# Optimization experiments

Hardware: AMD Instinct MI355X
Metric: run time of the kernel (lower is better)

## Reference

```python
import jax, jax.numpy as jnp
import numpy as np

DIM = 64; Hh = 128; Ww = 128; Bz = 4
N = 8      # d_state
R = 4      # dt_rank = ceil(dim/16)
K = 4      # depthwise conv kernel
NB = 4     # number of CrossMambaBlocks (spa, spe, spa_cross, spe_cross)


def setup_inputs() -> dict:
    key = jax.random.key(0)
    ks = jax.random.split(key, 16)
    f32 = jnp.float32
    D = DIM
    rn = lambda k, shp, s: jax.random.normal(k, shp, f32) * s
    inp = {
        "img1": rn(ks[0], (Bz, D, Hh, Ww), 1.0),
        "img2": rn(ks[1], (Bz, D, Hh, Ww), 1.0),
        "img1_sum": rn(ks[2], (Bz, D, Hh, Ww), 1.0),
        "img2_sum": rn(ks[3], (Bz, D, Hh, Ww), 1.0),
        # LayerNorm params for norm0/norm1 of each block
        "ln_g0": jnp.ones((NB, D), f32), "ln_b0": jnp.zeros((NB, D), f32),
        "ln_g1": jnp.ones((NB, D), f32), "ln_b1": jnp.zeros((NB, D), f32),
        # Mamba projections (in_proj -> x,z from input0; in_proj_e -> extra embedding path)
        "W_in": rn(ks[4], (NB, D, 2 * D), D ** -0.5),
        "W_ine": rn(ks[5], (NB, D, D), D ** -0.5),
        # per-direction depthwise causal conv
        "convW": rn(ks[6], (NB, 2, D, K), K ** -0.5),
        "convB": jnp.zeros((NB, 2, D), f32),
        # x_proj (dt, B, C) computed from the cross-modal embedding (v7 cross variant)
        "W_x": rn(ks[7], (NB, 2, D, R + 2 * N), D ** -0.5),
        "W_dt": rn(ks[8], (NB, 2, R, D), R ** -0.5),
        "b_dt": jnp.full((NB, 2, D), -4.6, f32),  # softplus ~ 0.01
        "A_log": jnp.log(jnp.broadcast_to(jnp.arange(1, N + 1, dtype=f32), (NB, 2, D, N))),
        "Dp": jnp.ones((NB, 2, D), f32),
        "W_out": rn(ks[9], (NB, D, D), D ** -0.5),
        "b_out": jnp.zeros((NB, D), f32),
        # FusionMamba.out_proj
        "W_fo": rn(ks[10], (D, D), D ** -0.5),
        "b_fo": jnp.zeros((D,), f32),
    }
    return inp


def _ln(x, g, b):
    m = x.mean(-1, keepdims=True)
    v = ((x - m) ** 2).mean(-1, keepdims=True)
    return (x - m) * jax.lax.rsqrt(v + 1e-5) * g + b


def _causal_conv(x, w, b):
    # x: [B, L, D], w: [D, K] depthwise causal conv
    xt = x.transpose(0, 2, 1)  # [B, D, L]
    out = jax.lax.conv_general_dilated(xt, w[:, None, :], (1,), [(K - 1, 0)],
                                       feature_group_count=w.shape[0])
    return out.transpose(0, 2, 1) + b


def _selective_scan(x, dt, Bm, Cm, A):
    # x, dt: [B, L, D]; Bm, Cm: [B, L, N]; A: [D, N]
    def step(h, t):
        x_t, dt_t, B_t, C_t = t  # [B,D],[B,D],[B,N],[B,N]
        dA = jnp.exp(dt_t[:, :, None] * A)                       # [B,D,N]
        h = h * dA + (dt_t * x_t)[:, :, None] * B_t[:, None, :]  # [B,D,N]
        y = jnp.einsum('bdn,bn->bd', h, C_t)
        return h, y
    h0 = jnp.zeros((x.shape[0], x.shape[2], A.shape[1]), x.dtype)
    xs = (x.transpose(1, 0, 2), dt.transpose(1, 0, 2),
          Bm.transpose(1, 0, 2), Cm.transpose(1, 0, 2))
    _, ys = jax.lax.scan(step, h0, xs)
    return ys.transpose(1, 0, 2)  # [B, L, D]


def _cross_mamba_block(x0, x1, i, p):
    # x0, x1: [B, L, D]; bidirectional cross Mamba (bimamba v7, sum of directions)
    skip = x0
    a = _ln(x0, p['ln_g0'][i], p['ln_b0'][i])
    e = _ln(x1, p['ln_g1'][i], p['ln_b1'][i])
    xz = a @ p['W_in'][i]
    x, z = jnp.split(xz, 2, axis=-1)
    ee = e @ p['W_ine'][i]  # cross-modal embedding drives dt/B/C
    y = 0.0
    for d in range(2):
        xd = x if d == 0 else x[:, ::-1]
        ed = ee if d == 0 else ee[:, ::-1]
        zd = z if d == 0 else z[:, ::-1]
        xc = jax.nn.silu(_causal_conv(xd, p['convW'][i, d], p['convB'][i, d]))
        dbl = ed @ p['W_x'][i, d]
        dtr, Bm, Cm = dbl[..., :R], dbl[..., R:R + N], dbl[..., R + N:]
        dt = jax.nn.softplus(dtr @ p['W_dt'][i, d] + p['b_dt'][i, d])
        A = -jnp.exp(p['A_log'][i, d])
        yd = _selective_scan(xc, dt, Bm, Cm, A) + xc * p['Dp'][i, d]
        yd = yd * jax.nn.silu(zd)
        if d == 1:
            yd = yd[:, ::-1]
        y = y + yd
    return y @ p['W_out'][i] + p['b_out'][i] + skip


def reference(img1, img2, img1_sum, img2_sum, ln_g0, ln_b0, ln_g1, ln_b1,
              W_in, W_ine, convW, convB, W_x, W_dt, b_dt, A_log, Dp,
              W_out, b_out, W_fo, b_fo):
    p = dict(ln_g0=ln_g0, ln_b0=ln_b0, ln_g1=ln_g1, ln_b1=ln_b1, W_in=W_in,
             W_ine=W_ine, convW=convW, convB=convB, W_x=W_x, W_dt=W_dt,
             b_dt=b_dt, A_log=A_log, Dp=Dp, W_out=W_out, b_out=b_out)
    b, c, h, w = img1.shape
    flat = lambda t: t.reshape(b, c, h * w).transpose(0, 2, 1)   # b c h w -> b (hw) c
    unflat = lambda t: t.transpose(0, 2, 1).reshape(b, c, h, w)
    x1, x2, s1, s2 = flat(img1), flat(img2), flat(img1_sum), flat(img2_sum)
    x1 = _cross_mamba_block(x1, s1, 0, p)  # spa layer
    x2 = _cross_mamba_block(x2, s2, 1, p)  # spe layer
    spa = _cross_mamba_block(x1, x2, 2, p)
    spe = _cross_mamba_block(x2, x1, 3, p)
    fusion = (spa + spe) @ W_fo + b_fo
    out = unflat(fusion)
    return (unflat(x1) + out, unflat(x2) + out, img1_sum, img2_sum)
```

## Files before the change

### kernel.cpp

```cpp
#include <hip/hip_runtime.h>
#include <hip/hip_bf16.h>

#define BZ 4
#define DD 64
#define LL 16384
#define NN 8
#define BLD ((size_t)BZ*DD*LL)
#define BML ((size_t)BZ*20*LL)

__device__ __forceinline__ float silu_(float x){ return __fdividef(x, 1.f + __expf(-x)); }
__device__ __forceinline__ float softplus_(float x){ return (x > 20.f) ? x : __logf(1.f + __expf(x)); }


__global__ __launch_bounds__(256)
void k_in2(const float* __restrict__ s0a, const float* __restrict__ s1a,
           const float* __restrict__ s0b, const float* __restrict__ s1b,
           const float* __restrict__ lng0, const float* __restrict__ lnb0,
           const float* __restrict__ lng1, const float* __restrict__ lnb1,
           const float* __restrict__ W_in, const float* __restrict__ W_ine,
           const float* __restrict__ W_x, int i0,
           float* __restrict__ XBa, float* __restrict__ ZBa,
           float* __restrict__ XBb, float* __restrict__ ZBb,
           float* __restrict__ M00, float* __restrict__ M01,
           float* __restrict__ M10, float* __restrict__ M11)
{
  const int sel  = blockIdx.x >> 8;
  const int pi   = sel / 3;
  const int role = sel - 3*pi;
  const int pos = (blockIdx.x & 255)*256 + threadIdx.x;
  const int b = pos >> 14;
  const int l = pos & (LL-1);
  const int i = i0 + pi;

  if (role < 2){
    const float* src0 = pi ? s0b : s0a;
    float a[DD];
    #pragma unroll
    for (int ch=0; ch<DD; ++ch) a[ch] = src0[((size_t)(b*DD+ch))*LL + l];
    float m=0.f;
    #pragma unroll
    for (int k=0;k<DD;++k) m += a[k];
    m *= (1.f/DD);
    float v=0.f;
    #pragma unroll
    for (int k=0;k<DD;++k){ float d=a[k]-m; v += d*d; }
    v *= (1.f/DD);
    const float rs = rsqrtf(v + 1e-5f);
    #pragma unroll
    for (int k=0;k<DD;++k) a[k] = (a[k]-m)*rs*lng0[i*DD+k] + lnb0[i*DD+k];

    const float* Wi = W_in + (size_t)i*DD*2*DD;
    float* drow = ((role==0) ? (pi ? XBb : XBa) : (pi ? ZBb : ZBa)) + ((size_t)b*LL + l)*DD;
    const int gbase = role*4;
    for (int g=0; g<4; ++g){
      float acc[16];
      #pragma unroll
      for (int j=0;j<16;++j) acc[j]=0.f;
      #pragma unroll
      for (int k=0;k<DD;++k){
        const float av = a[k];
        const float* wr = Wi + k*128 + (gbase+g)*16;
        #pragma unroll
        for (int j=0;j<16;++j) acc[j] = fmaf(av, wr[j], acc[j]);
      }
      #pragma unroll
      for (int q=0;q<4;++q)
        ((float4*)(drow + g*16))[q] = make_float4(acc[4*q],acc[4*q+1],acc[4*q+2],acc[4*q+3]);
    }
  } else {
    const float* src1 = pi ? s1b : s1a;
    float e[DD];
    #pragma unroll
    for (int ch=0; ch<DD; ++ch) e[ch] = src1[((size_t)(b*DD+ch))*LL + l];
    float m=0.f;
    #pragma unroll
    for (int k=0;k<DD;++k) m += e[k];
    m *= (1.f/DD);
    float v=0.f;
    #pragma unroll
    for (int k=0;k<DD;++k){ float d=e[k]-m; v += d*d; }
    v *= (1.f/DD);
    const float rs = rsqrtf(v + 1e-5f);
    #pragma unroll
    for (int k=0;k<DD;++k) e[k] = (e[k]-m)*rs*lng1[i*DD+k] + lnb1[i*DD+k];

    const float* We  = W_ine + (size_t)i*DD*DD;
    const float* Wx0 = W_x + ((size_t)(i*2+0)*DD)*20;
    const float* Wx1 = W_x + ((size_t)(i*2+1)*DD)*20;
    float acc0[20], acc1[20];
    #pragma unroll
    for (int j=0;j<20;++j){ acc0[j]=0.f; acc1[j]=0.f; }
    for (int gg=0; gg<4; ++gg){
      float eeg[16];
      #pragma unroll
      for (int j=0;j<16;++j) eeg[j]=0.f;
      #pragma unroll
      for (int k=0;k<DD;++k){
        const float ev = e[k];
        const float* wr = We + k*DD + gg*16;
        #pragma unroll
        for (int j=0;j<16;++j) eeg[j] = fmaf(ev, wr[j], eeg[j]);
      }
      const float* w0 = Wx0 + (size_t)(gg*16)*20;
      const float* w1 = Wx1 + (size_t)(gg*16)*20;
      #pragma unroll
      for (int jj=0;jj<16;++jj){
        const float s = eeg[jj];
        #pragma unroll
        for (int j=0;j<20;++j){
          acc0[j] = fmaf(s, w0[jj*20+j], acc0[j]);
          acc1[j] = fmaf(s, w1[jj*20+j], acc1[j]);
        }
      }
    }
    float* mrow0 = (pi ? M10 : M00) + ((size_t)b*LL + l)*20;
    float* mrow1 = (pi ? M11 : M01) + ((size_t)b*LL + l)*20;
    #pragma unroll
    for (int q=0;q<5;++q){
      ((float4*)mrow0)[q] = make_float4(acc0[4*q],acc0[4*q+1],acc0[4*q+2],acc0[4*q+3]);
      ((float4*)mrow1)[q] = make_float4(acc1[4*q],acc1[4*q+1],acc1[4*q+2],acc1[4*q+3]);
    }
  }
}

template<int NC2, bool PASSC>
__global__ __launch_bounds__(64)
void k_scan4(const float* __restrict__ XBa, const float* __restrict__ XBb,
             const float* __restrict__ ZBa, const float* __restrict__ ZBb,
             float* __restrict__ Y0, float* __restrict__ Y1,
             float* __restrict__ Y2, float* __restrict__ Y3,
             const float* __restrict__ M00, const float* __restrict__ M01,
             const float* __restrict__ M10, const float* __restrict__ M11,
             const float* __restrict__ convW, const float* __restrict__ convB,
             const float* __restrict__ Wdt, const float* __restrict__ bdt,
             const float* __restrict__ Alog, const float* __restrict__ Dpw, int i0,
             float* __restrict__ PP, float* __restrict__ FF,
             const float* __restrict__ HH)
{
  const int TC2 = LL / NC2;
  const size_t SC2 = (size_t)BZ*NC2*DD*NN;
  const int inst = blockIdx.x / (BZ*NC2);
  const int rb = blockIdx.x - inst*(BZ*NC2);
  const int c = rb & (NC2-1);
  const int b = rb / NC2;
  const int ch = threadIdx.x;
  const int pi = inst >> 1, d = inst & 1;
  const int id = (i0+pi)*2 + d;

  const float* xb = pi ? XBb : XBa;
  const float* zb = pi ? ZBb : ZBa;
  const float* meta = (inst==0)?M00:(inst==1)?M01:(inst==2)?M10:M11;
  float* yb = (inst==0)?Y0:(inst==1)?Y1:(inst==2)?Y2:Y3;

  float cw[4];
  #pragma unroll
  for (int k=0;k<4;++k) cw[k] = convW[((size_t)id*DD+ch)*4 + k];
  const float cb = convB[id*DD + ch];
  float wd[4];
  #pragma unroll
  for (int r=0;r<4;++r) wd[r] = Wdt[((size_t)id*4 + r)*DD + ch];
  const float bd = bdt[id*DD + ch];
  float An[NN];
  #pragma unroll
  for (int n=0;n<NN;++n) An[n] = -__expf(Alog[((size_t)id*DD+ch)*NN + n]);
  const float dp = PASSC ? Dpw[id*DD + ch] : 0.f;

  bool fastA = true;
  #pragma unroll
  for (int n=0;n<NN;++n) fastA = fastA && (fabsf(An[n] + (float)(n+1)) < 1e-3f);

  const size_t sbase = (size_t)inst*SC2 + ((size_t)(b*NC2+c)*DD + ch)*NN;
  float h[NN], P[NN];
  float Sdt = 0.f;
  if (PASSC){
    #pragma unroll
    for (int n=0;n<NN;++n) h[n] = HH[sbase+n];
  } else {
    #pragma unroll
    for (int n=0;n<NN;++n){ h[n]=0.f; P[n]=1.f; }
  }

  const int stp = d ? -1 : 1;
  const int t0  = d ? (LL-1 - c*TC2) : (c*TC2);

  float p1=0.f, p2=0.f, p3=0.f;
  {
    int tp = t0 - stp;
    if ((unsigned)tp < LL) p1 = xb[((size_t)b*LL+tp)*DD+ch];
    tp -= stp;
    if ((unsigned)tp < LL) p2 = xb[((size_t)b*LL+tp)*DD+ch];
    tp -= stp;
    if ((unsigned)tp < LL) p3 = xb[((size_t)b*LL+tp)*DD+ch];
  }

  int t = t0;
  for (int s=0; s<TC2; ++s, t+=stp){
    const size_t row = (size_t)b*LL + t;
    const float xv = xb[row*DD+ch];
    const float xc = silu_(cb + cw[0]*p3 + cw[1]*p2 + cw[2]*p1 + cw[3]*xv);
    p3=p2; p2=p1; p1=xv;

    const float* mt = meta + row*20;
    const float dpre = bd + mt[0]*wd[0] + mt[1]*wd[1] + mt[2]*wd[2] + mt[3]*wd[3];
    const float dt = softplus_(dpre);
    const float u = dt*xc;

    float dA[NN];
    if (fastA){
      const float E = __expf(-dt);
      const float E2 = E*E, E4 = E2*E2;
      dA[0]=E;    dA[1]=E2;    dA[2]=E2*E;  dA[3]=E4;
      dA[4]=E4*E; dA[5]=E4*E2; dA[6]=E4*E2*E; dA[7]=E4*E4;
      Sdt += dt;
    } else {
      #pragma unroll
      for (int n=0;n<NN;++n) dA[n] = __expf(dt*An[n]);
    }

    if (!PASSC){
      #pragma unroll
      for (int n=0;n<NN;++n) h[n] = fmaf(h[n], dA[n], u*mt[4+n]);
      if (!fastA){
        #pragma unroll
        for (int n=0;n<NN;++n) P[n] *= dA[n];
      }
    } else {
      float y = 0.f;
      #pragma unroll
      for (int n=0;n<NN;++n){
        h[n] = fmaf(h[n], dA[n], u*mt[4+n]);
        y = fmaf(h[n], mt[12+n], y);
      }
      const float zv = zb[row*DD+ch];
      yb[row*DD + ch] = (y + xc*dp)*silu_(zv);
    }
  }

  if (!PASSC){
    if (fastA){
      const float E = __expf(-Sdt);
      const float E2 = E*E, E4 = E2*E2;
      P[0]=E;    P[1]=E2;    P[2]=E2*E;  P[3]=E4;
      P[4]=E4*E; P[5]=E4*E2; P[6]=E4*E2*E; P[7]=E4*E4;
    }
    #pragma unroll
    for (int n=0;n<NN;++n){ PP[sbase+n] = P[n]; FF[sbase+n] = h[n]; }
  }
}

template<int NC2>
__global__ __launch_bounds__(256)
void k_mid4(const float* __restrict__ PP, const float* __restrict__ FF,
            float* __restrict__ HH)
{
  const size_t SC2 = (size_t)BZ*NC2*DD*NN;
  const int inst = blockIdx.x >> 3;
  const int idx = (blockIdx.x & 7)*256 + threadIdx.x;
  const int b  = idx >> 9;
  const int cn = idx & 511;
  const size_t base = (size_t)inst*SC2;
  float h = 0.f;
  #pragma unroll 4
  for (int c=0; c<NC2; ++c){
    const size_t a2 = base + (((size_t)(b*NC2+c))<<9) + cn;
    HH[a2] = h;
    h = h*PP[a2] + FF[a2];
  }
}

__global__ __launch_bounds__(256)
void k_out2(const float* __restrict__ Y0, const float* __restrict__ Y1,
            const float* __restrict__ Y2, const float* __restrict__ Y3,
            const float* __restrict__ skipA, const float* __restrict__ skipB,
            const float* __restrict__ Wout, const float* __restrict__ bout,
            float* __restrict__ dstA, float* __restrict__ dstB)
{
  const int sel = blockIdx.x >> 8;
  const int pi = sel >> 2;
  const int g  = sel & 3;
  const int pos = (blockIdx.x & 255)*256 + threadIdx.x;
  const int b = pos >> 14;
  const int l = pos & (LL-1);
  const size_t row = ((size_t)b*LL + l)*DD;

  const float* Ya = pi ? Y2 : Y0;
  const float* Yb = pi ? Y3 : Y1;
  const float* skip = pi ? skipB : skipA;
  float* dst = pi ? dstB : dstA;
  const float* Wo = Wout + (size_t)pi*DD*DD;
  const float* bo = bout + pi*DD;

  float y[DD];
  {
    const float4* pa = (const float4*)(Ya + row);
    const float4* pb = (const float4*)(Yb + row);
    #pragma unroll
    for (int q=0;q<16;++q){
      float4 v0=pa[q], v1=pb[q];
      y[4*q]=v0.x+v1.x; y[4*q+1]=v0.y+v1.y; y[4*q+2]=v0.z+v1.z; y[4*q+3]=v0.w+v1.w;
    }
  }
  float acc[16];
  #pragma unroll
  for (int j=0;j<16;++j) acc[j]=0.f;
  #pragma unroll
  for (int k=0;k<DD;++k){
    const float av = y[k];
    const float* wr = Wo + k*DD + g*16;
    #pragma unroll
    for (int j=0;j<16;++j) acc[j] = fmaf(av, wr[j], acc[j]);
  }
  #pragma unroll
  for (int j=0;j<16;++j){
    const int col = g*16 + j;
    const size_t o = ((size_t)(b*DD+col))*LL + l;
    dst[o] = acc[j] + bo[col] + skip[o];
  }
}

__global__ __launch_bounds__(256)
void k_o34(const float* __restrict__ Y0, const float* __restrict__ Y1,
           const float* __restrict__ Y2, const float* __restrict__ Y3,
           const float* __restrict__ X1, const float* __restrict__ X2,
           const float* __restrict__ Wout, const float* __restrict__ bout,
           float* __restrict__ FSa, float* __restrict__ FSb)
{
  const int sel = blockIdx.x >> 8;
  const int wh = sel >> 2;
  const int g  = sel & 3;
  const int pos = (blockIdx.x & 255)*256 + threadIdx.x;
  const int b = pos >> 14;
  const int l = pos & (LL-1);
  const size_t row = ((size_t)b*LL + l)*DD;

  const float* Ya = wh ? Y2 : Y0;
  const float* Yb = wh ? Y3 : Y1;
  const float* skip = wh ? X2 : X1;
  float* FS = wh ? FSb : FSa;
  const float* Wo = Wout + (size_t)(2+wh)*DD*DD;
  const float* bo = bout + (2+wh)*DD;

  float y[DD];
  {
    const float4* pa = (const float4*)(Ya + row);
    const float4* pb = (const float4*)(Yb + row);
    #pragma unroll
    for (int q=0;q<16;++q){
      float4 v0=pa[q], v1=pb[q];
      y[4*q]=v0.x+v1.x; y[4*q+1]=v0.y+v1.y; y[4*q+2]=v0.z+v1.z; y[4*q+3]=v0.w+v1.w;
    }
  }
  float acc[16];
  #pragma unroll
  for (int j=0;j<16;++j) acc[j]=0.f;
  #pragma unroll
  for (int k=0;k<DD;++k){
    const float av = y[k];
    const float* wr = Wo + k*DD + g*16;
    #pragma unroll
    for (int j=0;j<16;++j) acc[j] = fmaf(av, wr[j], acc[j]);
  }
  float* frow = FS + row + g*16;
  #pragma unroll
  for (int q=0;q<4;++q){
    const int j4 = 4*q;
    make_float4(0,0,0,0);
    float4 v;
    v.x = acc[j4+0] + bo[g*16+j4+0] + skip[((size_t)(b*DD+g*16+j4+0))*LL + l];
    v.y = acc[j4+1] + bo[g*16+j4+1] + skip[((size_t)(b*DD+g*16+j4+1))*LL + l];
    v.z = acc[j4+2] + bo[g*16+j4+2] + skip[((size_t)(b*DD+g*16+j4+2))*LL + l];
    v.w = acc[j4+3] + bo[g*16+j4+3] + skip[((size_t)(b*DD+g*16+j4+3))*LL + l];
    ((float4*)frow)[q] = v;
  }
}

__global__ __launch_bounds__(256)
void k_fuse2(const float* __restrict__ FSa, const float* __restrict__ FSb,
             const float* __restrict__ X1, const float* __restrict__ X2,
             const float* __restrict__ Wfo, const float* __restrict__ bfo,
             float* __restrict__ ob)
{
  const int g = blockIdx.x >> 8;
  const int pos = (blockIdx.x & 255)*256 + threadIdx.x;
  const int b = pos >> 14;
  const int l = pos & (LL-1);
  const size_t row = ((size_t)b*LL + l)*DD;

  float fs[DD];
  {
    const float4* pa = (const float4*)(FSa + row);
    const float4* pb = (const float4*)(FSb + row);
    #pragma unroll
    for (int q=0;q<16;++q){
      float4 v0=pa[q], v1=pb[q];
      fs[4*q]=v0.x+v1.x; fs[4*q+1]=v0.y+v1.y; fs[4*q+2]=v0.z+v1.z; fs[4*q+3]=v0.w+v1.w;
    }
  }
  float acc[16];
  #pragma unroll
  for (int j=0;j<16;++j) acc[j]=0.f;
  #pragma unroll
  for (int k=0;k<DD;++k){
    const float av = fs[k];
    const float* wr = Wfo + k*DD + g*16;
    #pragma unroll
    for (int j=0;j<16;++j) acc[j] = fmaf(av, wr[j], acc[j]);
  }
  #pragma unroll
  for (int j=0;j<16;++j){
    const int col = g*16 + j;
    const size_t o = ((size_t)(b*DD+col))*LL + l;
    const float fu = acc[j] + bfo[col];
    ob[o]       = X1[o] + fu;
    ob[BLD + o] = X2[o] + fu;
  }
}

__global__ __launch_bounds__(256)
void k_copyboth(const float* __restrict__ s1, const float* __restrict__ s2,
                float* __restrict__ o)
{
  const size_t gid = (size_t)blockIdx.x*256 + threadIdx.x;
  const size_t half = BLD/4;
  if (gid < half) ((float4*)(o        ))[gid]        = ((const float4*)s1)[gid];
  else            ((float4*)(o + BLD ))[gid - half]  = ((const float4*)s2)[gid - half];
}

__global__ __launch_bounds__(256)
void k_copy4(const float* __restrict__ s, float* __restrict__ o)
{
  const size_t i = (size_t)blockIdx.x*256 + threadIdx.x;
  ((float4*)o)[i] = ((const float4*)s)[i];
}

__global__ __launch_bounds__(256)
void f_in(const float* __restrict__ src0, const float* __restrict__ src1,
          const float* __restrict__ lng0, const float* __restrict__ lnb0,
          const float* __restrict__ lng1, const float* __restrict__ lnb1,
          const float* __restrict__ W_in, const float* __restrict__ W_ine,
          const float* __restrict__ W_x, int i,
          float* __restrict__ XB, float* __restrict__ ZB,
          float* __restrict__ M0, float* __restrict__ M1)
{
  const int gid = blockIdx.x*256 + threadIdx.x;
  const int b = gid >> 14;
  const int l = gid & (LL-1);

  float a[DD];
  for (int ch=0; ch<DD; ++ch) a[ch] = src0[((size_t)(b*DD+ch))*LL + l];
  {
    float m=0.f; for (int k=0;k<DD;++k) m += a[k];  m *= (1.f/DD);
    float v=0.f; for (int k=0;k<DD;++k){ float d=a[k]-m; v += d*d; }  v *= (1.f/DD);
    float rs = rsqrtf(v + 1e-5f);
    for (int k=0;k<DD;++k) a[k] = (a[k]-m)*rs*lng0[i*DD+k] + lnb0[i*DD+k];
  }
  const float* Wi = W_in + (size_t)i*DD*2*DD;
  float* xrow = XB + ((size_t)b*LL + l)*DD;
  float* zrow = ZB + ((size_t)b*LL + l)*DD;
  for (int g=0; g<8; ++g){
    float acc[16];
    #pragma unroll
    for (int j=0;j<16;++j) acc[j]=0.f;
    for (int k=0;k<DD;++k){
      const float av = a[k];
      const float* wr = Wi + k*128 + g*16;
      #pragma unroll
      for (int j=0;j<16;++j) acc[j] = fmaf(av, wr[j], acc[j]);
    }
    float* drow = (g<4) ? (xrow + g*16) : (zrow + (g-4)*16);
    #pragma unroll
    for (int q=0;q<4;++q)
      ((float4*)drow)[q] = make_float4(acc[4*q],acc[4*q+1],acc[4*q+2],acc[4*q+3]);
  }
  float e[DD], ee[DD];
  for (int ch=0; ch<DD; ++ch) e[ch] = src1[((size_t)(b*DD+ch))*LL + l];
  {
    float m=0.f; for (int k=0;k<DD;++k) m += e[k];  m *= (1.f/DD);
    float v=0.f; for (int k=0;k<DD;++k){ float d=e[k]-m; v += d*d; }  v *= (1.f/DD);
    float rs = rsqrtf(v + 1e-5f);
    for (int k=0;k<DD;++k) e[k] = (e[k]-m)*rs*lng1[i*DD+k] + lnb1[i*DD+k];
  }
  const float* We = W_ine + (size_t)i*DD*DD;
  for (int m2=0; m2<DD; ++m2){
    float s = 0.f;
    for (int k=0;k<DD;++k) s = fmaf(e[k], We[k*DD + m2], s);
    ee[m2] = s;
  }
  for (int d=0; d<2; ++d){
    float acc[20];
    #pragma unroll
    for (int j=0;j<20;++j) acc[j]=0.f;
    for (int m2=0; m2<DD; ++m2){
      const float ev = ee[m2];
      const float* wr = W_x + ((size_t)(i*2+d)*DD + m2)*20;
      #pragma unroll
      for (int j=0;j<20;++j) acc[j] = fmaf(ev, wr[j], acc[j]);
    }
    float* mrow = (d ? M1 : M0) + ((size_t)b*LL + l)*20;
    #pragma unroll
    for (int q=0;q<5;++q)
      ((float4*)mrow)[q] = make_float4(acc[4*q],acc[4*q+1],acc[4*q+2],acc[4*q+3]);
  }
}

template<int DIR, bool PASSC>
__global__ __launch_bounds__(64)
void f_scan(const float* __restrict__ xb, const float* __restrict__ zb,
            float* __restrict__ yb, const float* __restrict__ meta,
            const float* __restrict__ convW, const float* __restrict__ convB,
            const float* __restrict__ Wdt, const float* __restrict__ bdt,
            const float* __restrict__ Alog, const float* __restrict__ Dpw, int id,
            float* __restrict__ Pb, float* __restrict__ Fb,
            const float* __restrict__ Hin)
{
  const int ch = threadIdx.x;
  const int c  = blockIdx.x & 255;
  const int b  = blockIdx.x >> 8;

  float cw[4];
  for (int k=0;k<4;++k) cw[k] = convW[((size_t)id*DD+ch)*4 + k];
  const float cb = convB[id*DD + ch];
  float wd[4]; for (int r=0;r<4;++r) wd[r] = Wdt[((size_t)id*4 + r)*DD + ch];
  const float bd = bdt[id*DD + ch];
  float An[NN]; for (int n=0;n<NN;++n) An[n] = -__expf(Alog[((size_t)id*DD+ch)*NN + n]);
  const float dp = PASSC ? Dpw[id*DD + ch] : 0.f;

  const size_t sbase = ((size_t)(b*256+c)*DD + ch)*NN;
  float h[NN], P[NN];
  if (PASSC){
    #pragma unroll
    for (int n=0;n<NN;++n) h[n] = Hin[sbase+n];
  } else {
    #pragma unroll
    for (int n=0;n<NN;++n){ h[n]=0.f; P[n]=1.f; }
  }

  int t0, stp;
  if (DIR==0){ t0 = c*64;        stp =  1; }
  else       { t0 = LL-1 - c*64; stp = -1; }

  float p1=0.f, p2=0.f, p3=0.f;
  {
    int tp = t0 - stp;
    if ((unsigned)tp < LL) p1 = xb[((size_t)b*LL+tp)*DD+ch];
    tp -= stp;
    if ((unsigned)tp < LL) p2 = xb[((size_t)b*LL+tp)*DD+ch];
    tp -= stp;
    if ((unsigned)tp < LL) p3 = xb[((size_t)b*LL+tp)*DD+ch];
  }

  int t = t0;
  for (int s=0; s<64; ++s, t+=stp){
    const size_t row = (size_t)b*LL + t;
    const float xv = xb[row*DD+ch];
    const float xc = silu_(cb + cw[0]*p3 + cw[1]*p2 + cw[2]*p1 + cw[3]*xv);
    p3=p2; p2=p1; p1=xv;

    const float* mt = meta + row*20;
    const float dpre = bd + mt[0]*wd[0] + mt[1]*wd[1] + mt[2]*wd[2] + mt[3]*wd[3];
    const float dt = softplus_(dpre);
    const float u = dt*xc;

    if (!PASSC){
      #pragma unroll
      for (int n=0;n<NN;++n){
        const float dA = __expf(dt*An[n]);
        h[n] = h[n]*dA + u*mt[4+n];
        P[n] *= dA;
      }
    } else {
      float y = 0.f;
      #pragma unroll
      for (int n=0;n<NN;++n){
        const float dA = __expf(dt*An[n]);
        h[n] = h[n]*dA + u*mt[4+n];
        y = fmaf(h[n], mt[12+n], y);
      }
      const float zv = zb[row*DD+ch];
      const float o = (y + xc*dp)*silu_(zv);
      float* yp = yb + row*DD + ch;
      if (DIR==0) *yp = o; else *yp += o;
    }
  }

  if (!PASSC){
    #pragma unroll
    for (int n=0;n<NN;++n){ Pb[sbase+n] = P[n]; Fb[sbase+n] = h[n]; }
  }
}

__global__ __launch_bounds__(256)
void f_mid(const float* __restrict__ Pb, const float* __restrict__ Fb,
           float* __restrict__ Hin)
{
  const int idx = blockIdx.x*256 + threadIdx.x;
  const int b  = idx >> 9;
  const int cn = idx & 511;
  float h = 0.f;
  #pragma unroll 4
  for (int c=0; c<256; ++c){
    const size_t a2 = (((size_t)(b*256+c))<<9) + cn;
    Hin[a2] = h;
    h = h*Pb[a2] + Fb[a2];
  }
}

template<int MODE>
__global__ __launch_bounds__(256)
void f_out(const float* __restrict__ YB, const float* __restrict__ skip,
           const float* __restrict__ Wo, const float* __restrict__ bo,
           float* __restrict__ dst)
{
  const int gid = blockIdx.x*256 + threadIdx.x;
  const int b = gid >> 14;
  const int l = gid & (LL-1);
  float y[DD];
  {
    const float4* s4 = (const float4*)(YB + ((size_t)b*LL + l)*DD);
    #pragma unroll
    for (int q=0;q<16;++q){ float4 v=s4[q]; y[4*q]=v.x; y[4*q+1]=v.y; y[4*q+2]=v.z; y[4*q+3]=v.w; }
  }
  for (int g=0; g<4; ++g){
    float acc[16];
    #pragma unroll
    for (int j=0;j<16;++j) acc[j]=0.f;
    for (int k=0;k<DD;++k){
      const float av = y[k];
      const float* wr = Wo + k*DD + g*16;
      #pragma unroll
      for (int j=0;j<16;++j) acc[j] = fmaf(av, wr[j], acc[j]);
    }
    #pragma unroll
    for (int j=0;j<16;++j){
      const int col = g*16 + j;
      const size_t o = ((size_t)(b*DD+col))*LL + l;
      float s = acc[j] + bo[col] + skip[o];
      if (MODE==1) s += dst[o];
      dst[o] = s;
    }
  }
}

__global__ __launch_bounds__(256)
void f_fuse(const float* __restrict__ FS, const float* __restrict__ X1,
            const float* __restrict__ X2, const float* __restrict__ Wfo,
            const float* __restrict__ bfo, float* __restrict__ ob)
{
  const int gid = blockIdx.x*256 + threadIdx.x;
  const int b = gid >> 14;
  const int l = gid & (LL-1);
  float fs[DD];
  for (int ch=0; ch<DD; ++ch) fs[ch] = FS[((size_t)(b*DD+ch))*LL + l];
  for (int g=0; g<4; ++g){
    float acc[16];
    #pragma unroll
    for (int j=0;j<16;++j) acc[j]=0.f;
    for (int k=0;k<DD;++k){
      const float av = fs[k];
      const float* wr = Wfo + k*DD + g*16;
      #pragma unroll
      for (int j=0;j<16;++j) acc[j] = fmaf(av, wr[j], acc[j]);
    }
    #pragma unroll
    for (int j=0;j<16;++j){
      const int col = g*16 + j;
      const size_t o = ((size_t)(b*DD+col))*LL + l;
      const float fu = acc[j] + bfo[col];
      ob[o]       = X1[o] + fu;
      ob[BLD + o] = X2[o] + fu;
    }
  }
}

extern "C" void kernel_launch(void* const* d_in, const int* in_sizes, int n_in,
                              void* d_out, int out_size, void* d_ws, size_t ws_size,
                              hipStream_t stream)
{
  static const int dictsz[21]  = {4194304,4194304,4194304,4194304,256,256,256,256,
                                  32768,16384,2048,512,10240,2048,512,4096,512,
                                  16384,256,4096,64};
  int map[21];
  bool okd = (n_in >= 21);
  if (okd) for (int i=0;i<21;++i) if (in_sizes[i] != dictsz[i]) { okd = false; break; }
  if (okd){
    for (int i=0;i<21;++i) map[i] = i;
  } else {
    bool used[64];
    for (int j=0;j<64;++j) used[j]=false;
    for (int i=0;i<21;++i){
      map[i] = -1;
      for (int j=0;j<n_in && j<64;++j)
        if (!used[j] && in_sizes[j]==dictsz[i]){ map[i]=j; used[j]=true; break; }
      if (map[i] < 0) map[i] = (i < n_in ? i : 0);
    }
  }

  const float* img1 = (const float*)d_in[map[0]];
  const float* img2 = (const float*)d_in[map[1]];
  const float* s1   = (const float*)d_in[map[2]];
  const float* s2   = (const float*)d_in[map[3]];
  const float* lng0 = (const float*)d_in[map[4]];
  const float* lnb0 = (const float*)d_in[map[5]];
  const float* lng1 = (const float*)d_in[map[6]];
  const float* lnb1 = (const float*)d_in[map[7]];
  const float* Win  = (const float*)d_in[map[8]];
  const float* Wine = (const float*)d_in[map[9]];
  const float* convW= (const float*)d_in[map[10]];
  const float* convB= (const float*)d_in[map[11]];
  const float* Wx   = (const float*)d_in[map[12]];
  const float* Wdt  = (const float*)d_in[map[13]];
  const float* bdt  = (const float*)d_in[map[14]];
  const float* Alog = (const float*)d_in[map[15]];
  const float* Dp   = (const float*)d_in[map[16]];
  const float* Wout = (const float*)d_in[map[17]];
  const float* bout = (const float*)d_in[map[18]];
  const float* Wfo  = (const float*)d_in[map[19]];
  const float* bfo  = (const float*)d_in[map[20]];

  float* ob = (float*)d_out;
  float* ws = (float*)d_ws;

  const size_t SCN512 = (size_t)BZ*512*DD*NN;
  const size_t SCN256 = (size_t)BZ*256*DD*NN;
  const size_t need512 = (10*BLD + 4*BML + 12*SCN512 + 64)*sizeof(float);
  const size_t need256 = (10*BLD + 4*BML + 12*SCN256 + 64)*sizeof(float);

  if (ws_size >= need256){
    k_copyboth<<<8192,256,0,stream>>>(s1, s2, ob + 2*BLD);

    const bool big = (ws_size >= need512);
    const size_t SC = big ? SCN512 : SCN256;
    float* X1  = ws;
    float* X2  = ws + 1*BLD;
    float* XBa = ws + 2*BLD;
    float* ZBa = ws + 3*BLD;
    float* XBb = ws + 4*BLD;
    float* ZBb = ws + 5*BLD;
    float* Y0  = ws + 6*BLD;
    float* Y1  = ws + 7*BLD;
    float* Y2  = ws + 8*BLD;
    float* Y3  = ws + 9*BLD;
    float* M00 = ws + 10*BLD;
    float* M01 = M00 + BML;
    float* M10 = M01 + BML;
    float* M11 = M10 + BML;
    float* PP  = M11 + BML;
    float* FF  = PP + 4*SC;
    float* HH  = FF + 4*SC;

    for (int pr=0; pr<2; ++pr){
      const int i0 = pr*2;
      if (pr==0)
        k_in2<<<1536,256,0,stream>>>(img1, s1, img2, s2, lng0,lnb0,lng1,lnb1,
                                     Win, Wine, Wx, 0, XBa,ZBa,XBb,ZBb, M00,M01,M10,M11);
      else
        k_in2<<<1536,256,0,stream>>>(X1, X2, X2, X1, lng0,lnb0,lng1,lnb1,
                                     Win, Wine, Wx, 2, XBa,ZBa,XBb,ZBb, M00,M01,M10,M11);
      if (big){
        k_scan4<512,false><<<4*BZ*512,64,0,stream>>>(XBa,XBb,ZBa,ZBb, Y0,Y1,Y2,Y3,
                                                     M00,M01,M10,M11, convW,convB,Wdt,bdt,Alog,Dp,
                                                     i0, PP,FF,HH);
        k_mid4<512><<<32,256,0,stream>>>(PP,FF,HH);
        k_scan4<512,true ><<<4*BZ*512,64,0,stream>>>(XBa,XBb,ZBa,ZBb, Y0,Y1,Y2,Y3,
                                                     M00,M01,M10,M11, convW,convB,Wdt,bdt,Alog,Dp,
                                                     i0, PP,FF,HH);
      } else {
        k_scan4<256,false><<<4*BZ*256,64,0,stream>>>(XBa,XBb,ZBa,ZBb, Y0,Y1,Y2,Y3,
                                                     M00,M01,M10,M11, convW,convB,Wdt,bdt,Alog,Dp,
                                                     i0, PP,FF,HH);
        k_mid4<256><<<32,256,0,stream>>>(PP,FF,HH);
        k_scan4<256,true ><<<4*BZ*256,64,0,stream>>>(XBa,XBb,ZBa,ZBb, Y0,Y1,Y2,Y3,
                                                     M00,M01,M10,M11, convW,convB,Wdt,bdt,Alog,Dp,
                                                     i0, PP,FF,HH);
      }
      if (pr==0){
        k_out2<<<2048,256,0,stream>>>(Y0,Y1,Y2,Y3, img1,img2, Wout,bout, X1,X2);
      } else {
        k_o34<<<2048,256,0,stream>>>(Y0,Y1,Y2,Y3, X1,X2, Wout,bout, XBa, ZBa);
        k_fuse2<<<1024,256,0,stream>>>(XBa, ZBa, X1, X2, Wfo, bfo, ob);
      }
    }
    return;
  }

  k_copy4<<<4096,256,0,stream>>>(s1, ob + 2*BLD);
  k_copy4<<<4096,256,0,stream>>>(s2, ob + 3*BLD);

  float* X1 = ws;
  float* X2 = ws + 1*BLD;
  float* FS = ws + 2*BLD;
  float* XB = ws + 3*BLD;
  float* ZB = ws + 4*BLD;
  float* YB = ws + 5*BLD;
  float* M0 = ws + 6*BLD;
  float* M1 = M0 + BML;
  float* PP = M1 + BML;
  float* FF = PP + SCN256;
  float* HH = FF + SCN256;

  const size_t need = (6*BLD + 2*BML + 3*SCN256 + 64)*sizeof(float);
  if (ws_size < need) return;

  const float* bx0[4] = {img1, img2, X1, X2};
  const float* bx1[4] = {s1,   s2,   X2, X1};

  for (int i=0; i<4; ++i){
    f_in<<<256,256,0,stream>>>(bx0[i], bx1[i], lng0, lnb0, lng1, lnb1,
                               Win, Wine, Wx, i, XB, ZB, M0, M1);
    for (int d=0; d<2; ++d){
      const int id = i*2+d;
      const float* Md = d ? M1 : M0;
      if (d==0){
        f_scan<0,false><<<BZ*256,64,0,stream>>>(XB,nullptr,nullptr,Md,convW,convB,Wdt,bdt,Alog,nullptr,id,PP,FF,nullptr);
        f_mid<<<8,256,0,stream>>>(PP,FF,HH);
        f_scan<0,true ><<<BZ*256,64,0,stream>>>(XB,ZB,YB,Md,convW,convB,Wdt,bdt,Alog,Dp,id,nullptr,nullptr,HH);
      } else {
        f_scan<1,false><<<BZ*256,64,0,stream>>>(XB,nullptr,nullptr,Md,convW,convB,Wdt,bdt,Alog,nullptr,id,PP,FF,nullptr);
        f_mid<<<8,256,0,stream>>>(PP,FF,HH);
        f_scan<1,true ><<<BZ*256,64,0,stream>>>(XB,ZB,YB,Md,convW,convB,Wdt,bdt,Alog,Dp,id,nullptr,nullptr,HH);
      }
    }
    const float* Wop = Wout + (size_t)i*DD*DD;
    const float* bop = bout + (size_t)i*DD;
    if      (i==0) f_out<0><<<256,256,0,stream>>>(YB, img1, Wop, bop, X1);
    else if (i==1) f_out<0><<<256,256,0,stream>>>(YB, img2, Wop, bop, X2);
    else if (i==2) f_out<0><<<256,256,0,stream>>>(YB, X1,   Wop, bop, FS);
    else           f_out<1><<<256,256,0,stream>>>(YB, X2,   Wop, bop, FS);
  }
  f_fuse<<<256,256,0,stream>>>(FS, X1, X2, Wfo, bfo, ob);
}
```

Before: 821.4 us.

## Transpose inputs to token-major once and use row-wise float4 loads everywhere

Adds a shared-memory transpose kernel that converts img1, img2 and both sum tensors from channel-major to token-major layout before the pipeline. k_in2, k_out2, k_o34 and k_fuse2 then read and write activations as contiguous per-token rows with float4 accesses instead of one strided channel-major access per channel. X1 and X2 are now held token-major in the workspace, and Y0 and Y1 are reused as scratch for the transposed sum inputs. The cost is an extra full read and write pass over four input tensors. The old strided accesses were already coalesced across threads, so the new layout may gain little.

```diff
diff --git a/kernel.cpp b/kernel.cpp
--- a/kernel.cpp
+++ b/kernel.cpp
@@ -11,6 +11,34 @@
 __device__ __forceinline__ float silu_(float x){ return __fdividef(x, 1.f + __expf(-x)); }
 __device__ __forceinline__ float softplus_(float x){ return (x > 20.f) ? x : __logf(1.f + __expf(x)); }
 
+
+__global__ __launch_bounds__(256)
+void k_tr(const float* __restrict__ t0, const float* __restrict__ t1,
+          const float* __restrict__ t2, const float* __restrict__ t3,
+          float* __restrict__ d0, float* __restrict__ d1,
+          float* __restrict__ d2, float* __restrict__ d3)
+{
+  __shared__ float tile[64][65];
+  const int tid = blockIdx.x;
+  const int tsr = tid >> 10;
+  const int rem = tid & 1023;
+  const int b  = rem >> 8;
+  const int l0 = (rem & 255) << 6;
+  const float* s = (tsr==0)?t0:(tsr==1)?t1:(tsr==2)?t2:t3;
+  float*       d = (tsr==0)?d0:(tsr==1)?d1:(tsr==2)?d2:d3;
+  const int w = threadIdx.x >> 6, lane = threadIdx.x & 63;
+  #pragma unroll
+  for (int i=0;i<16;++i){
+    const int ch = w*16+i;
+    tile[ch][lane] = s[((size_t)(b*DD+ch))*LL + l0 + lane];
+  }
+  __syncthreads();
+  #pragma unroll
+  for (int i=0;i<16;++i){
+    const int lw = w*16+i;
+    d[((size_t)b*LL + l0+lw)*DD + lane] = tile[lane][lw];
+  }
+}
 
 __global__ __launch_bounds__(256)
 void k_in2(const float* __restrict__ s0a, const float* __restrict__ s1a,
@@ -31,12 +59,16 @@
   const int b = pos >> 14;
   const int l = pos & (LL-1);
   const int i = i0 + pi;
+  const size_t row = ((size_t)b*LL + l)*DD;
 
   if (role < 2){
     const float* src0 = pi ? s0b : s0a;
     float a[DD];
-    #pragma unroll
-    for (int ch=0; ch<DD; ++ch) a[ch] = src0[((size_t)(b*DD+ch))*LL + l];
+    {
+      const float4* s4 = (const float4*)(src0 + row);
+      #pragma unroll
+      for (int q=0;q<16;++q){ float4 v=s4[q]; a[4*q]=v.x; a[4*q+1]=v.y; a[4*q+2]=v.z; a[4*q+3]=v.w; }
+    }
     float m=0.f;
     #pragma unroll
     for (int k=0;k<DD;++k) m += a[k];
@@ -50,7 +82,7 @@
     for (int k=0;k<DD;++k) a[k] = (a[k]-m)*rs*lng0[i*DD+k] + lnb0[i*DD+k];
 
     const float* Wi = W_in + (size_t)i*DD*2*DD;
-    float* drow = ((role==0) ? (pi ? XBb : XBa) : (pi ? ZBb : ZBa)) + ((size_t)b*LL + l)*DD;
+    float* drow = ((role==0) ? (pi ? XBb : XBa) : (pi ? ZBb : ZBa)) + row;
     const int gbase = role*4;
     for (int g=0; g<4; ++g){
       float acc[16];
@@ -70,8 +102,11 @@
   } else {
     const float* src1 = pi ? s1b : s1a;
     float e[DD];
-    #pragma unroll
-    for (int ch=0; ch<DD; ++ch) e[ch] = src1[((size_t)(b*DD+ch))*LL + l];
+    {
+      const float4* s4 = (const float4*)(src1 + row);
+      #pragma unroll
+      for (int q=0;q<16;++q){ float4 v=s4[q]; e[4*q]=v.x; e[4*q+1]=v.y; e[4*q+2]=v.z; e[4*q+3]=v.w; }
+    }
     float m=0.f;
     #pragma unroll
     for (int k=0;k<DD;++k) m += e[k];
@@ -310,11 +345,17 @@
     #pragma unroll
     for (int j=0;j<16;++j) acc[j] = fmaf(av, wr[j], acc[j]);
   }
-  #pragma unroll
-  for (int j=0;j<16;++j){
-    const int col = g*16 + j;
-    const size_t o = ((size_t)(b*DD+col))*LL + l;
-    dst[o] = acc[j] + bo[col] + skip[o];
+  const float4* sk4 = (const float4*)(skip + row + g*16);
+  float4* d4 = (float4*)(dst + row + g*16);
+  #pragma unroll
+  for (int q=0;q<4;++q){
+    float4 sv = sk4[q];
+    float4 v;
+    v.x = acc[4*q+0] + bo[g*16+4*q+0] + sv.x;
+    v.y = acc[4*q+1] + bo[g*16+4*q+1] + sv.y;
+    v.z = acc[4*q+2] + bo[g*16+4*q+2] + sv.z;
+    v.w = acc[4*q+3] + bo[g*16+4*q+3] + sv.w;
+    d4[q] = v;
   }
 }
 
@@ -360,17 +401,17 @@
     #pragma unroll
     for (int j=0;j<16;++j) acc[j] = fmaf(av, wr[j], acc[j]);
   }
-  float* frow = FS + row + g*16;
+  const float4* sk4 = (const float4*)(skip + row + g*16);
+  float4* f4 = (float4*)(FS + row + g*16);
   #pragma unroll
   for (int q=0;q<4;++q){
-    const int j4 = 4*q;
-    make_float4(0,0,0,0);
+    float4 sv = sk4[q];
     float4 v;
-    v.x = acc[j4+0] + bo[g*16+j4+0] + skip[((size_t)(b*DD+g*16+j4+0))*LL + l];
-    v.y = acc[j4+1] + bo[g*16+j4+1] + skip[((size_t)(b*DD+g*16+j4+1))*LL + l];
-    v.z = acc[j4+2] + bo[g*16+j4+2] + skip[((size_t)(b*DD+g*16+j4+2))*LL + l];
-    v.w = acc[j4+3] + bo[g*16+j4+3] + skip[((size_t)(b*DD+g*16+j4+3))*LL + l];
-    ((float4*)frow)[q] = v;
+    v.x = acc[4*q+0] + bo[g*16+4*q+0] + sv.x;
+    v.y = acc[4*q+1] + bo[g*16+4*q+1] + sv.y;
+    v.z = acc[4*q+2] + bo[g*16+4*q+2] + sv.z;
+    v.w = acc[4*q+3] + bo[g*16+4*q+3] + sv.w;
+    f4[q] = v;
   }
 }
 
@@ -406,13 +447,24 @@
     #pragma unroll
     for (int j=0;j<16;++j) acc[j] = fmaf(av, wr[j], acc[j]);
   }
+  float x1v[16], x2v[16];
+  {
+    const float4* p1 = (const float4*)(X1 + row + g*16);
+    const float4* p2 = (const float4*)(X2 + row + g*16);
+    #pragma unroll
+    for (int q=0;q<4;++q){
+      float4 v1=p1[q], v2=p2[q];
+      x1v[4*q]=v1.x; x1v[4*q+1]=v1.y; x1v[4*q+2]=v1.z; x1v[4*q+3]=v1.w;
+      x2v[4*q]=v2.x; x2v[4*q+1]=v2.y; x2v[4*q+2]=v2.z; x2v[4*q+3]=v2.w;
+    }
+  }
   #pragma unroll
   for (int j=0;j<16;++j){
     const int col = g*16 + j;
     const size_t o = ((size_t)(b*DD+col))*LL + l;
     const float fu = acc[j] + bfo[col];
-    ob[o]       = X1[o] + fu;
-    ob[BLD + o] = X2[o] + fu;
+    ob[o]       = x1v[j] + fu;
+    ob[BLD + o] = x2v[j] + fu;
   }
 }
 
@@ -748,10 +800,12 @@
     float* FF  = PP + 4*SC;
     float* HH  = FF + 4*SC;
 
+    k_tr<<<4096,256,0,stream>>>(img1, img2, s1, s2, X1, X2, Y0, Y1);
+
     for (int pr=0; pr<2; ++pr){
       const int i0 = pr*2;
       if (pr==0)
-        k_in2<<<1536,256,0,stream>>>(img1, s1, img2, s2, lng0,lnb0,lng1,lnb1,
+        k_in2<<<1536,256,0,stream>>>(X1, Y0, X2, Y1, lng0,lnb0,lng1,lnb1,
                                      Win, Wine, Wx, 0, XBa,ZBa,XBb,ZBb, M00,M01,M10,M11);
       else
         k_in2<<<1536,256,0,stream>>>(X1, X2, X2, X1, lng0,lnb0,lng1,lnb1,
@@ -774,7 +828,7 @@
                                                      i0, PP,FF,HH);
       }
       if (pr==0){
-        k_out2<<<2048,256,0,stream>>>(Y0,Y1,Y2,Y3, img1,img2, Wout,bout, X1,X2);
+        k_out2<<<2048,256,0,stream>>>(Y0,Y1,Y2,Y3, X1,X2, Wout,bout, X1,X2);
       } else {
         k_o34<<<2048,256,0,stream>>>(Y0,Y1,Y2,Y3, X1,X2, Wout,bout, XBa, ZBa);
         k_fuse2<<<1024,256,0,stream>>>(XBa, ZBa, X1, X2, Wfo, bfo, ob);
```

New measurement: 857.3 us. 4.4% more time.
